# Kernel optimization log

Measured on AMD Instinct MI355X. Metric: run time of the kernel, lower is better.

Reference implementation:

```python
import jax, jax.numpy as jnp
import numpy as np

NUM_NODES = 100000
INPUT_DIM = 256
NUM_BAGS = 2048
BAG_SIZE = 64
N_EDGES = 3200000  # num_nodes * avg_degree(32)


def setup_inputs() -> dict:
    key = jax.random.key(0)
    ks = jax.random.split(key, 7)
    x = jax.random.normal(ks[0], (NUM_NODES, INPUT_DIM), dtype=jnp.float32)
    bags = jax.random.randint(ks[1], (NUM_BAGS, BAG_SIZE), 0, NUM_NODES)
    alpha_values = jax.random.uniform(ks[2], (NUM_BAGS, BAG_SIZE, 1), dtype=jnp.float32)
    # edge_dict in COO form: edge_src[e] has neighbor edge_nbr[e]
    edge_src = jax.random.randint(ks[3], (N_EDGES,), 0, NUM_NODES)
    edge_nbr = jax.random.randint(ks[4], (N_EDGES,), 0, NUM_NODES)
    node_weights = jax.random.uniform(ks[5], (NUM_NODES,), dtype=jnp.float32)  # torch.rand init
    theta_w = jax.random.normal(ks[6], (INPUT_DIM,), dtype=jnp.float32) / np.sqrt(INPUT_DIM)
    return dict(x=x, bags=bags, alpha_values=alpha_values, edge_src=edge_src,
                edge_nbr=edge_nbr, node_weights=node_weights, theta_w=theta_w)


def reference(x, bags, alpha_values, edge_src, edge_nbr, node_weights, theta_w):
    # Per-source neighbor weight sum: sum_value(source) = sum(node_weights[edge_dict[source]])
    nbr_sum = jax.ops.segment_sum(node_weights[edge_nbr], edge_src, num_segments=NUM_NODES)
    deg = jax.ops.segment_sum(jnp.ones_like(edge_src, dtype=x.dtype), edge_src,
                              num_segments=NUM_NODES)
    # sources not in edge_dict get sum_value = 1.0
    nbr_sum = jnp.where(deg > 0, nbr_sum, jnp.asarray(1.0, x.dtype))
    # h_values = theta(x[bag]); theta is Linear(input_dim, 1, bias=False)
    h = jnp.einsum('nbd,d->nb', x[bags], theta_w)          # [num_bags, bag_size]
    feat = h * alpha_values[..., 0]                         # [num_bags, bag_size]
    ns = nbr_sum[bags]                                      # [num_bags, bag_size]
    return jnp.sum(ns * feat, axis=1)                       # [num_bags]
```

## Files before the change

kernel.cpp:

```cpp
#include <hip/hip_runtime.h>

#define NUM_NODES 100000
#define INPUT_DIM 256
#define NUM_BAGS  2048
#define BAG_SIZE  64
#define N_EDGES   3200000
#define NQUAD     (N_EDGES / 4)
#define P_PART    8
#define NPP       12500
#define NSLICE    32
#define QPS       (NQUAD / NSLICE)

typedef unsigned int u32;
typedef float f4 __attribute__((ext_vector_type(4)));

__global__ void __launch_bounds__(256)
pack_edges(const int* __restrict__ edge_src, const int* __restrict__ edge_nbr,
           const float* __restrict__ nw, u32* __restrict__ packed) {
    const int q = blockIdx.x * 256 + threadIdx.x;
    const int4 s4 = ((const int4*)edge_src)[q];
    const int4 n4 = ((const int4*)edge_nbr)[q];
#define PACK(S, N)  (((u32)(S) << 15) |                                     \
                     (((__float_as_uint(nw[(N)]) + 0x8000u) >> 16) & 0x7FFFu))
    uint4 o;
    o.x = PACK(s4.x, n4.x);
    o.y = PACK(s4.y, n4.y);
    o.z = PACK(s4.z, n4.z);
    o.w = PACK(s4.w, n4.w);
#undef PACK
    ((uint4*)packed)[q] = o;
}

__global__ void __launch_bounds__(1024)
hist_p(const u32* __restrict__ packed, float* __restrict__ rep) {
    __shared__ float hist[NPP];
    const int i    = blockIdx.x;
    const int r    = i & 7;
    const int p    = (i >> 3) & 7;
    const int b    = r | ((i >> 6) << 3);
    const int base = p * NPP;

    for (int j = threadIdx.x; j < NPP / 4; j += 1024)
        ((f4*)hist)[j] = (f4){0.f, 0.f, 0.f, 0.f};
    __syncthreads();

    const int lo  = b * QPS;
    const int tid = threadIdx.x;

#define EDGE(W)                                                          \
        {                                                                \
            const u32 rel = ((W) >> 15) - (u32)base;                     \
            if (rel < (u32)NPP)                                          \
                atomicAdd(&hist[rel],                                    \
                          __uint_as_float(((W) & 0x7FFFu) << 16));       \
        }
    #pragma unroll 2
    for (int it = 0; it < 12; ++it) {
        const int q0 = lo + it * 2048 + tid;
        const uint4 a = ((const uint4*)packed)[q0];
        const uint4 c = ((const uint4*)packed)[q0 + 1024];
        EDGE(a.x) EDGE(a.y) EDGE(a.z) EDGE(a.w)
        EDGE(c.x) EDGE(c.y) EDGE(c.z) EDGE(c.w)
    }
    if (tid < 424) {
        const uint4 a = ((const uint4*)packed)[lo + 24576 + tid];
        EDGE(a.x) EDGE(a.y) EDGE(a.z) EDGE(a.w)
    }
#undef EDGE
    __syncthreads();

    float* dst = rep + (size_t)b * NUM_NODES + base;
    for (int j = threadIdx.x; j < NPP / 4; j += 1024) {
        const f4 v = ((const f4*)hist)[j];
        __builtin_nontemporal_store(v, &((f4*)dst)[j]);
    }
}

#define RED_BLK 98
__global__ void __launch_bounds__(256)
gemv_reduce(const float* __restrict__ rep, float* __restrict__ nbr_sum,
            const float* __restrict__ x, const float* __restrict__ theta,
            float* __restrict__ h) {
    if (blockIdx.x < RED_BLK) {
        const int i = blockIdx.x * 256 + threadIdx.x;
        if (i >= NUM_NODES / 4) return;
        float4 a = make_float4(0.f, 0.f, 0.f, 0.f);
        #pragma unroll 8
        for (int r = 0; r < NSLICE; ++r) {
            const float4 v = ((const float4*)(rep + (size_t)r * NUM_NODES))[i];
            a.x += v.x; a.y += v.y; a.z += v.z; a.w += v.w;
        }
        float4 o;
        o.x = a.x > 0.f ? a.x : 1.0f;
        o.y = a.y > 0.f ? a.y : 1.0f;
        o.z = a.z > 0.f ? a.z : 1.0f;
        o.w = a.w > 0.f ? a.w : 1.0f;
        ((float4*)nbr_sum)[i] = o;
    } else {
        const int gb   = blockIdx.x - RED_BLK;
        const int lane = threadIdx.x & 63;
        const int wave = threadIdx.x >> 6;
        const float4 tw = *reinterpret_cast<const float4*>(&theta[lane * 4]);
        for (int row = gb * 4 + wave; row < NUM_NODES; row += 2048 * 4) {
            const float4 xv =
                *reinterpret_cast<const float4*>(&x[(size_t)row * INPUT_DIM + lane * 4]);
            float d = xv.x * tw.x + xv.y * tw.y + xv.z * tw.z + xv.w * tw.w;
            #pragma unroll
            for (int off = 32; off >= 1; off >>= 1)
                d += __shfl_xor(d, off);
            if (lane == 0) h[row] = d;
        }
    }
}

__global__ void __launch_bounds__(256)
bag_final(const int* __restrict__ bags, const float* __restrict__ alpha,
          const float* __restrict__ h, const float* __restrict__ ns,
          float* __restrict__ out) {
    const int bag  = blockIdx.x * 4 + (threadIdx.x >> 6);
    const int lane = threadIdx.x & 63;
    const int idx  = bags[bag * BAG_SIZE + lane];
    float v = h[idx] * ns[idx] * alpha[bag * BAG_SIZE + lane];
    #pragma unroll
    for (int off = 32; off >= 1; off >>= 1)
        v += __shfl_xor(v, off);
    if (lane == 0) out[bag] = v;
}

__global__ void __launch_bounds__(256)
edge_atomic(const int* __restrict__ edge_src, const int* __restrict__ edge_nbr,
            const float* __restrict__ nw, float* __restrict__ nbr_sum) {
    const int t = blockIdx.x * blockDim.x + threadIdx.x;
    const int4 s4 = ((const int4*)edge_src)[t];
    const int4 n4 = ((const int4*)edge_nbr)[t];
    atomicAdd(&nbr_sum[s4.x], nw[n4.x]);
    atomicAdd(&nbr_sum[s4.y], nw[n4.y]);
    atomicAdd(&nbr_sum[s4.z], nw[n4.z]);
    atomicAdd(&nbr_sum[s4.w], nw[n4.w]);
}

__global__ void __launch_bounds__(256)
fixup_nosum(float* __restrict__ nbr_sum) {
    const int i = blockIdx.x * 256 + threadIdx.x;
    if (i < NUM_NODES && nbr_sum[i] == 0.f) nbr_sum[i] = 1.0f;
}

__global__ void __launch_bounds__(256)
gemv_h(const float* __restrict__ x, const float* __restrict__ theta,
       float* __restrict__ h) {
    const int lane = threadIdx.x & 63;
    const int wave = threadIdx.x >> 6;
    const float4 tw = *reinterpret_cast<const float4*>(&theta[lane * 4]);
    const int stride = gridDim.x * 4;
    for (int row = blockIdx.x * 4 + wave; row < NUM_NODES; row += stride) {
        const float4 xv =
            *reinterpret_cast<const float4*>(&x[(size_t)row * INPUT_DIM + lane * 4]);
        float d = xv.x * tw.x + xv.y * tw.y + xv.z * tw.z + xv.w * tw.w;
        #pragma unroll
        for (int off = 32; off >= 1; off >>= 1)
            d += __shfl_xor(d, off);
        if (lane == 0) h[row] = d;
    }
}

extern "C" void kernel_launch(void* const* d_in, const int* in_sizes, int n_in,
                              void* d_out, int out_size, void* d_ws, size_t ws_size,
                              hipStream_t stream) {
    const float* x            = (const float*)d_in[0];
    const int*   bags         = (const int*)d_in[1];
    const float* alpha        = (const float*)d_in[2];
    const int*   edge_src     = (const int*)d_in[3];
    const int*   edge_nbr     = (const int*)d_in[4];
    const float* node_weights = (const float*)d_in[5];
    const float* theta        = (const float*)d_in[6];
    float*       out          = (float*)d_out;

    const size_t need_full =
        ((size_t)N_EDGES + (size_t)NSLICE * NUM_NODES + 2 * (size_t)NUM_NODES) * 4;

    if (ws_size >= need_full) {
        u32*   packed  = (u32*)d_ws;
        float* rep     = (float*)d_ws + N_EDGES;
        float* nbr_sum = rep + (size_t)NSLICE * NUM_NODES;
        float* h       = nbr_sum + NUM_NODES;

        pack_edges<<<NQUAD / 256, 256, 0, stream>>>(edge_src, edge_nbr,
                                                    node_weights, packed);
        hist_p<<<P_PART * NSLICE, 1024, 0, stream>>>(packed, rep);
        gemv_reduce<<<RED_BLK + 2048, 256, 0, stream>>>(rep, nbr_sum, x, theta, h);
        bag_final<<<NUM_BAGS / 4, 256, 0, stream>>>(bags, alpha, h, nbr_sum, out);
    } else {
        float* nbr_sum = (float*)d_ws;
        float* h       = nbr_sum + NUM_NODES;
        hipMemsetAsync(nbr_sum, 0, (size_t)NUM_NODES * 4, stream);
        edge_atomic<<<(N_EDGES / 4) / 256, 256, 0, stream>>>(
            edge_src, edge_nbr, node_weights, nbr_sum);
        fixup_nosum<<<(NUM_NODES + 255) / 256, 256, 0, stream>>>(nbr_sum);
        gemv_h<<<2048, 256, 0, stream>>>(x, theta, h);
        bag_final<<<NUM_BAGS / 4, 256, 0, stream>>>(bags, alpha, h, nbr_sum, out);
    }
}
```

Measured before the change: 66.92 us.

## Use three large LDS node partitions with 85 edge slices for histogram

```diff
diff --git a/kernel.cpp b/kernel.cpp
--- a/kernel.cpp
+++ b/kernel.cpp
@@ -6,10 +6,13 @@
 #define BAG_SIZE  64
 #define N_EDGES   3200000
 #define NQUAD     (N_EDGES / 4)
-#define P_PART    8
-#define NPP       12500
-#define NSLICE    32
-#define QPS       (NQUAD / NSLICE)
+
+#define NPP3      33334
+#define NSL3      85
+#define QPS3      9412
+#define NPP8      12500
+#define NSL8      32
+#define QPS8      (NQUAD / NSL8)
 
 typedef unsigned int u32;
 typedef float f4 __attribute__((ext_vector_type(4)));
@@ -32,51 +35,75 @@
 }
 
 __global__ void __launch_bounds__(1024)
+hist3(const u32* __restrict__ packed, float* __restrict__ rep) {
+    extern __shared__ float hist[];
+    const int p    = blockIdx.x / NSL3;
+    const int b    = blockIdx.x % NSL3;
+    const int base = p * NPP3;
+    const int tid  = threadIdx.x;
+
+    for (int j = tid; j < NPP3; j += 1024) hist[j] = 0.f;
+    __syncthreads();
+
+    const int lo = b * QPS3;
+    const int hi = (lo + QPS3 < NQUAD) ? lo + QPS3 : NQUAD;
+#define EDGE(W)                                                          \
+        {                                                                \
+            const u32 rel = ((W) >> 15) - (u32)base;                     \
+            if (rel < (u32)NPP3)                                         \
+                atomicAdd(&hist[rel],                                    \
+                          __uint_as_float(((W) & 0x7FFFu) << 16));       \
+        }
+    for (int q = lo + tid; q < hi; q += 1024) {
+        const uint4 a = ((const uint4*)packed)[q];
+        EDGE(a.x) EDGE(a.y) EDGE(a.z) EDGE(a.w)
+    }
+#undef EDGE
+    __syncthreads();
+
+    const int nflush = (NUM_NODES - base < NPP3) ? NUM_NODES - base : NPP3;
+    float* dst = rep + (size_t)b * NUM_NODES + base;
+    for (int j = tid; j < nflush; j += 1024)
+        __builtin_nontemporal_store(hist[j], &dst[j]);
+}
+
+__global__ void __launch_bounds__(1024)
 hist_p(const u32* __restrict__ packed, float* __restrict__ rep) {
-    __shared__ float hist[NPP];
+    __shared__ float hist[NPP8];
     const int i    = blockIdx.x;
     const int r    = i & 7;
     const int p    = (i >> 3) & 7;
     const int b    = r | ((i >> 6) << 3);
-    const int base = p * NPP;
-
-    for (int j = threadIdx.x; j < NPP / 4; j += 1024)
+    const int base = p * NPP8;
+
+    for (int j = threadIdx.x; j < NPP8 / 4; j += 1024)
         ((f4*)hist)[j] = (f4){0.f, 0.f, 0.f, 0.f};
     __syncthreads();
 
-    const int lo  = b * QPS;
-    const int tid = threadIdx.x;
-
+    const int lo = b * QPS8;
 #define EDGE(W)                                                          \
         {                                                                \
             const u32 rel = ((W) >> 15) - (u32)base;                     \
-            if (rel < (u32)NPP)                                          \
+            if (rel < (u32)NPP8)                                         \
                 atomicAdd(&hist[rel],                                    \
                           __uint_as_float(((W) & 0x7FFFu) << 16));       \
         }
-    #pragma unroll 2
-    for (int it = 0; it < 12; ++it) {
-        const int q0 = lo + it * 2048 + tid;
-        const uint4 a = ((const uint4*)packed)[q0];
-        const uint4 c = ((const uint4*)packed)[q0 + 1024];
+    for (int q = lo + (int)threadIdx.x; q < lo + QPS8; q += 1024) {
+        const uint4 a = ((const uint4*)packed)[q];
         EDGE(a.x) EDGE(a.y) EDGE(a.z) EDGE(a.w)
-        EDGE(c.x) EDGE(c.y) EDGE(c.z) EDGE(c.w)
-    }
-    if (tid < 424) {
-        const uint4 a = ((const uint4*)packed)[lo + 24576 + tid];
-        EDGE(a.x) EDGE(a.y) EDGE(a.z) EDGE(a.w)
     }
 #undef EDGE
     __syncthreads();
 
     float* dst = rep + (size_t)b * NUM_NODES + base;
-    for (int j = threadIdx.x; j < NPP / 4; j += 1024) {
+    for (int j = threadIdx.x; j < NPP8 / 4; j += 1024) {
         const f4 v = ((const f4*)hist)[j];
         __builtin_nontemporal_store(v, &((f4*)dst)[j]);
     }
 }
 
 #define RED_BLK 98
+template <int NSL>
 __global__ void __launch_bounds__(256)
 gemv_reduce(const float* __restrict__ rep, float* __restrict__ nbr_sum,
             const float* __restrict__ x, const float* __restrict__ theta,
@@ -85,8 +112,8 @@
         const int i = blockIdx.x * 256 + threadIdx.x;
         if (i >= NUM_NODES / 4) return;
         float4 a = make_float4(0.f, 0.f, 0.f, 0.f);
-        #pragma unroll 8
-        for (int r = 0; r < NSLICE; ++r) {
+        #pragma unroll 5
+        for (int r = 0; r < NSL; ++r) {
             const float4 v = ((const float4*)(rep + (size_t)r * NUM_NODES))[i];
             a.x += v.x; a.y += v.y; a.z += v.z; a.w += v.w;
         }
@@ -175,19 +202,38 @@
     const float* theta        = (const float*)d_in[6];
     float*       out          = (float*)d_out;
 
-    const size_t need_full =
-        ((size_t)N_EDGES + (size_t)NSLICE * NUM_NODES + 2 * (size_t)NUM_NODES) * 4;
-
-    if (ws_size >= need_full) {
+    const size_t need3 =
+        ((size_t)N_EDGES + (size_t)NSL3 * NUM_NODES + 2 * (size_t)NUM_NODES) * 4;
+    const size_t need8 =
+        ((size_t)N_EDGES + (size_t)NSL8 * NUM_NODES + 2 * (size_t)NUM_NODES) * 4;
+
+    const hipError_t attr_ok = hipFuncSetAttribute(
+        (const void*)hist3, hipFuncAttributeMaxDynamicSharedMemorySize,
+        NPP3 * (int)sizeof(float));
+
+    if (attr_ok == hipSuccess && ws_size >= need3) {
         u32*   packed  = (u32*)d_ws;
         float* rep     = (float*)d_ws + N_EDGES;
-        float* nbr_sum = rep + (size_t)NSLICE * NUM_NODES;
+        float* nbr_sum = rep + (size_t)NSL3 * NUM_NODES;
         float* h       = nbr_sum + NUM_NODES;
 
         pack_edges<<<NQUAD / 256, 256, 0, stream>>>(edge_src, edge_nbr,
                                                     node_weights, packed);
-        hist_p<<<P_PART * NSLICE, 1024, 0, stream>>>(packed, rep);
-        gemv_reduce<<<RED_BLK + 2048, 256, 0, stream>>>(rep, nbr_sum, x, theta, h);
+        hist3<<<3 * NSL3, 1024, NPP3 * sizeof(float), stream>>>(packed, rep);
+        gemv_reduce<NSL3><<<RED_BLK + 2048, 256, 0, stream>>>(rep, nbr_sum,
+                                                              x, theta, h);
+        bag_final<<<NUM_BAGS / 4, 256, 0, stream>>>(bags, alpha, h, nbr_sum, out);
+    } else if (ws_size >= need8) {
+        u32*   packed  = (u32*)d_ws;
+        float* rep     = (float*)d_ws + N_EDGES;
+        float* nbr_sum = rep + (size_t)NSL8 * NUM_NODES;
+        float* h       = nbr_sum + NUM_NODES;
+
+        pack_edges<<<NQUAD / 256, 256, 0, stream>>>(edge_src, edge_nbr,
+                                                    node_weights, packed);
+        hist_p<<<8 * NSL8, 1024, 0, stream>>>(packed, rep);
+        gemv_reduce<NSL8><<<RED_BLK + 2048, 256, 0, stream>>>(rep, nbr_sum,
+                                                              x, theta, h);
         bag_final<<<NUM_BAGS / 4, 256, 0, stream>>>(bags, alpha, h, nbr_sum, out);
     } else {
         float* nbr_sum = (float*)d_ws;
```

Result: slower. 73.96 us (+10.5%).
